# Performance work log

Measured on AMD Instinct MI355X. Metric: run time of the kernel, lower is better.

Reference implementation:

```python
import jax, jax.numpy as jnp
import numpy as np

N = 100000   # nodes
E = 1600000  # edges (avg degree 16)
F_IN = 128   # num_features
H = 128      # num_hidden
C = 40       # num_classes


def setup_inputs() -> dict:
    key = jax.random.key(0)
    ks = jax.random.split(key, 8)
    w = lambda k, sh: jax.random.normal(k, sh, dtype=jnp.float32) * 0.05
    return {
        "x": jax.random.normal(ks[0], (N, F_IN), dtype=jnp.float32),
        "edge_index": jax.random.randint(ks[1], (2, E), 0, N),
        "W_rel1": w(ks[2], (F_IN, H)),
        "b_rel1": jnp.zeros((H,), jnp.float32),
        "W_root1": w(ks[3], (F_IN, H)),
        "W_rel2": w(ks[4], (H, H)),
        "b_rel2": jnp.zeros((H,), jnp.float32),
        "W_root2": w(ks[5], (H, H)),
        "W_lin": w(ks[6], (2 * H, C)),
        "b_lin": jnp.zeros((C,), jnp.float32),
    }


def _graph_conv(x, src, dst, W_rel, b_rel, W_root, n):
    # PyG GraphConv: sum_{j in N(i)} x_j -> lin_rel, plus lin_root(x_i)
    agg = jax.ops.segment_sum(x[src], dst, num_segments=n)  # [N, d_in]
    return agg @ W_rel + b_rel + x @ W_root


def reference(x, edge_index, W_rel1, b_rel1, W_root1, W_rel2, b_rel2, W_root2, W_lin, b_lin):
    src, dst = edge_index[0], edge_index[1]
    n = x.shape[0]
    # dropout is identity at inference (training=False)
    x1 = jax.nn.relu(_graph_conv(x, src, dst, W_rel1, b_rel1, W_root1, n))
    x2 = jax.nn.relu(_graph_conv(x1, src, dst, W_rel2, b_rel2, W_root2, n))
    h = jnp.concatenate([x1, x2], axis=-1)  # [N, 2H]
    return jax.nn.log_softmax(h @ W_lin + b_lin, axis=-1)
```

## Files before the change

kernel.cpp:

```cpp
#include <hip/hip_runtime.h>
#include <hip/hip_bf16.h>

typedef __attribute__((ext_vector_type(8))) short bf16x8;
typedef __attribute__((ext_vector_type(4))) float f32x4;
typedef __attribute__((ext_vector_type(2))) float f32x2;

#define EPB 4096
#define BUCKET_BITS 8
#define BUCKET_SIZE 256
#define MAXBUCK 512

static __device__ __forceinline__ unsigned short f2bf(float f) {
    union { float f; unsigned u; } v; v.f = f;
    unsigned r = v.u + 0x7FFF + ((v.u >> 16) & 1);
    return (unsigned short)(r >> 16);
}
static __device__ __forceinline__ float asf(unsigned u) {
    union { unsigned u; float f; } v; v.u = u;
    return v.f;
}
static __device__ __forceinline__ f32x2 cvt2(unsigned u) {
    f32x2 r;
    r.x = asf(u << 16);
    r.y = asf(u & 0xFFFF0000u);
    return r;
}

__global__ __launch_bounds__(256) void prep(const float* __restrict__ Wrel1,
                                            const float* __restrict__ Wroot1,
                                            const float* __restrict__ Wrel2,
                                            const float* __restrict__ Wroot2,
                                            const float* __restrict__ Wlin,
                                            const int* __restrict__ dst,
                                            unsigned short* __restrict__ bsw1,
                                            unsigned short* __restrict__ bsw2,
                                            unsigned short* __restrict__ bswL,
                                            int* __restrict__ hist,
                                            int E, int nblk, int nbuck) {
    __shared__ int h[MAXBUCK];
    int blk = blockIdx.x, t = threadIdx.x;
    if (blk < 256) {
        const float* Wrel  = (blk < 128) ? Wrel1 : Wrel2;
        const float* Wroot = (blk < 128) ? Wroot1 : Wroot2;
        unsigned short* bsw = (blk < 128) ? bsw1 : bsw2;
        int idx = (blk & 127) * 256 + t;
        int j = idx & 7, L = (idx >> 3) & 63, ct = (idx >> 9) & 15, kt = idx >> 13;
        int k = kt * 32 + ((L >> 4) * 8) + j;
        int c = ct * 16 + (L & 15);
        float v = (c < 128) ? Wrel[k * 128 + c] : Wroot[k * 128 + (c - 128)];
        bsw[idx] = f2bf(v);
    } else if (blk < 304) {
        int idx = (blk - 256) * 256 + t;
        int tt = idx;
        int j = tt & 7; tt >>= 3;
        int L = tt & 63; tt >>= 6;
        int ct = tt % 3;
        int kt = tt / 3;
        int k = kt * 32 + ((L >> 4) * 8) + j;
        int c = ct * 16 + (L & 15);
        float v = (c < 40) ? Wlin[k * 40 + c] : 0.f;
        bswL[idx] = f2bf(v);
    } else {
        int hb = blk - 304;
        for (int i = t; i < MAXBUCK; i += 256) h[i] = 0;
        __syncthreads();
        int e0 = hb * EPB;
#pragma unroll
        for (int it = 0; it < EPB / 256; it++) {
            int e = e0 + it * 256 + t;
            if (e < E) atomicAdd(&h[dst[e] >> BUCKET_BITS], 1);
        }
        __syncthreads();
        for (int i = t; i < nbuck; i += 256) hist[i * nblk + hb] = h[i];
    }
}

__global__ __launch_bounds__(256) void bucket_total(const int* __restrict__ hist,
                                                    int* __restrict__ total, int nblk) {
    __shared__ int s[256];
    int b = blockIdx.x, t = threadIdx.x;
    int v = 0;
    for (int i = t; i < nblk; i += 256) v += hist[b * nblk + i];
    s[t] = v; __syncthreads();
#pragma unroll
    for (int o = 128; o >= 1; o >>= 1) {
        if (t < o) s[t] += s[t + o];
        __syncthreads();
    }
    if (t == 0) total[b] = s[0];
}

__global__ __launch_bounds__(256) void bucket_scan(const int* __restrict__ total,
                                                   int* __restrict__ base, int nbuck) {
    __shared__ int s[256];
    int t = threadIdx.x;
    int e0 = (2 * t < nbuck) ? total[2 * t] : 0;
    int e1 = (2 * t + 1 < nbuck) ? total[2 * t + 1] : 0;
    int ps = e0 + e1;
    s[t] = ps; __syncthreads();
#pragma unroll
    for (int o = 1; o < 256; o <<= 1) {
        int x = (t >= o) ? s[t - o] : 0;
        __syncthreads();
        s[t] += x; __syncthreads();
    }
    int pbase = s[t] - ps;
    if (2 * t <= nbuck) base[2 * t] = pbase;
    if (2 * t + 1 <= nbuck) base[2 * t + 1] = pbase + e0;
}

__global__ __launch_bounds__(256) void block_scan(int* __restrict__ hist,
                                                  const int* __restrict__ base, int nblk) {
    __shared__ int s[256];
    int b = blockIdx.x, t = threadIdx.x;
    int carryv = base[b];
    for (int start = 0; start < nblk; start += 256) {
        int i = start + t;
        int v = (i < nblk) ? hist[b * nblk + i] : 0;
        s[t] = v; __syncthreads();
#pragma unroll
        for (int o = 1; o < 256; o <<= 1) {
            int x = (t >= o) ? s[t - o] : 0;
            __syncthreads();
            s[t] += x; __syncthreads();
        }
        int excl = s[t] - v + carryv;
        if (i < nblk) hist[b * nblk + i] = excl;
        carryv += s[255];
        __syncthreads();
    }
}

__global__ __launch_bounds__(256) void edge_part(const int* __restrict__ src,
                                                 const int* __restrict__ dst,
                                                 const int* __restrict__ hist,
                                                 int* __restrict__ part,
                                                 int E, int nblk, int nbuck) {
    __shared__ int hcnt[MAXBUCK];
    __shared__ int lstart[MAXBUCK];
    __shared__ int cur[MAXBUCK];
    __shared__ int gbase[MAXBUCK];
    __shared__ int s2[256];
    __shared__ int sdst[EPB];
    __shared__ int ssrc[EPB];
    int t = threadIdx.x, blk = blockIdx.x;
    int e0 = blk * EPB;
    int cnt = E - e0; if (cnt > EPB) cnt = EPB;
    for (int i = t; i < MAXBUCK; i += 256) hcnt[i] = 0;
    for (int i = t; i < nbuck; i += 256) gbase[i] = hist[i * nblk + blk];
    __syncthreads();
    int myd[EPB / 256], mys[EPB / 256];
#pragma unroll
    for (int it = 0; it < EPB / 256; it++) {
        int i = it * 256 + t;
        if (i < cnt) {
            myd[it] = dst[e0 + i];
            mys[it] = src[e0 + i];
            atomicAdd(&hcnt[myd[it] >> BUCKET_BITS], 1);
        }
    }
    __syncthreads();
    int p0 = hcnt[2 * t], p1 = hcnt[2 * t + 1];
    int ps = p0 + p1;
    s2[t] = ps; __syncthreads();
#pragma unroll
    for (int o = 1; o < 256; o <<= 1) {
        int x = (t >= o) ? s2[t - o] : 0;
        __syncthreads();
        s2[t] += x; __syncthreads();
    }
    int pbase = s2[t] - ps;
    lstart[2 * t] = pbase; lstart[2 * t + 1] = pbase + p0;
    cur[2 * t] = 0; cur[2 * t + 1] = 0;
    __syncthreads();
#pragma unroll
    for (int it = 0; it < EPB / 256; it++) {
        int i = it * 256 + t;
        if (i < cnt) {
            int b = myd[it] >> BUCKET_BITS;
            int p = lstart[b] + atomicAdd(&cur[b], 1);
            sdst[p] = myd[it];
            ssrc[p] = mys[it];
        }
    }
    __syncthreads();
    for (int i = t; i < cnt; i += 256) {
        int d = sdst[i], s = ssrc[i];
        int b = d >> BUCKET_BITS;
        part[gbase[b] + (i - lstart[b])] = ((d & (BUCKET_SIZE - 1)) << 17) | s;
    }
}

__global__ __launch_bounds__(256) void csrfin_gemm1(const int* __restrict__ part,
                                                    const int* __restrict__ bucketBase,
                                                    int* __restrict__ off_,
                                                    int* __restrict__ deg_,
                                                    int* __restrict__ csr_src,
                                                    const float* __restrict__ x,
                                                    const unsigned short* __restrict__ Bsw,
                                                    const float* __restrict__ bias,
                                                    unsigned short* __restrict__ xr,
                                                    unsigned short* __restrict__ accbf,
                                                    int N, int nbuck) {
    __shared__ int cur[BUCKET_SIZE];
    __shared__ int h[BUCKET_SIZE];
    __shared__ int tsum[256];
    int t = threadIdx.x;
    if (blockIdx.x < (unsigned)nbuck) {
        int b = blockIdx.x;
        int lo = bucketBase[b], hi = bucketBase[b + 1];
        int n0 = b * BUCKET_SIZE;
        h[t] = 0;
        __syncthreads();
        for (int i = lo + t; i < hi; i += 256) atomicAdd(&h[part[i] >> 17], 1);
        __syncthreads();
        int hv = h[t];
        tsum[t] = hv;
        __syncthreads();
#pragma unroll
        for (int o = 1; o < 256; o <<= 1) {
            int xx = (t >= o) ? tsum[t - o] : 0;
            __syncthreads();
            tsum[t] += xx;
            __syncthreads();
        }
        int st = tsum[t] - hv;
        cur[t] = st;
        int node = n0 + t;
        if (node < N) { off_[node] = lo + st; deg_[node] = hv; }
        __syncthreads();
        for (int i = lo + t; i < hi; i += 256) {
            int rec = part[i];
            int p = atomicAdd(&cur[rec >> 17], 1);
            csr_src[lo + p] = rec & 0x1FFFF;
        }
    } else {
        int wid = (blockIdx.x - nbuck) * 4 + (t >> 6);
        int L = t & 63;
        int r0 = wid * 16;
        if (r0 >= N) return;
        int arow = r0 + (L & 15);
        const bf16x8* Bptr = ((const bf16x8*)Bsw) + L;
        f32x4 acc[16];
#pragma unroll
        for (int i = 0; i < 16; i++) acc[i] = (f32x4){0.f, 0.f, 0.f, 0.f};
#pragma unroll
        for (int kt = 0; kt < 4; kt++) {
            const float* Arow = x + (size_t)arow * 128 + ((L >> 4) * 8) + kt * 32;
            float4 a0 = *(const float4*)Arow;
            float4 a1 = *(const float4*)(Arow + 4);
            bf16x8 a;
            a[0] = (short)f2bf(a0.x); a[1] = (short)f2bf(a0.y);
            a[2] = (short)f2bf(a0.z); a[3] = (short)f2bf(a0.w);
            a[4] = (short)f2bf(a1.x); a[5] = (short)f2bf(a1.y);
            a[6] = (short)f2bf(a1.z); a[7] = (short)f2bf(a1.w);
#pragma unroll
            for (int ct = 0; ct < 16; ct++) {
                bf16x8 b = Bptr[(kt * 16 + ct) * 64];
                acc[ct] = __builtin_amdgcn_mfma_f32_16x16x32_bf16(a, b, acc[ct], 0, 0, 0);
            }
        }
        int rbase = r0 + (L >> 4) * 4;
        int cl = L & 15;
#pragma unroll
        for (int ct = 0; ct < 16; ct++) {
            int col = ct * 16 + cl;
#pragma unroll
            for (int r = 0; r < 4; r++) {
                int row = rbase + r;
                float v = acc[ct][r];
                if (col < 128)
                    xr[(size_t)row * 128 + col] = f2bf(v);
                else
                    accbf[(size_t)row * 128 + (col - 128)] = f2bf(v + bias[col - 128]);
            }
        }
    }
}

__global__ __launch_bounds__(256) void gemm_layer2(const unsigned short* __restrict__ Abf,
                                                   const unsigned short* __restrict__ Bsw,
                                                   const float* __restrict__ bias,
                                                   unsigned short* __restrict__ xr,
                                                   unsigned short* __restrict__ accbf, int N) {
    __shared__ unsigned short Bs[32768];
    int t = threadIdx.x;
    {
        uint4* d4 = (uint4*)Bs;
        const uint4* s4 = (const uint4*)Bsw;
#pragma unroll
        for (int i = 0; i < 16; i++) d4[t + i * 256] = s4[t + i * 256];
    }
    __syncthreads();
    int w = t >> 6, L = t & 63;
    int nTiles = (N + 15) / 16;
    for (int tile = blockIdx.x * 4 + w; tile < nTiles; tile += gridDim.x * 4) {
        int r0 = tile * 16;
        int arow = r0 + (L & 15);
        f32x4 acc[16];
#pragma unroll
        for (int i = 0; i < 16; i++) acc[i] = (f32x4){0.f, 0.f, 0.f, 0.f};
#pragma unroll
        for (int kt = 0; kt < 4; kt++) {
            bf16x8 a = *((const bf16x8*)(Abf + (size_t)arow * 128 + ((L >> 4) * 8) + kt * 32));
#pragma unroll
            for (int ct = 0; ct < 16; ct++) {
                bf16x8 b = *(const bf16x8*)(Bs + (((kt * 16 + ct) * 64) + L) * 8);
                acc[ct] = __builtin_amdgcn_mfma_f32_16x16x32_bf16(a, b, acc[ct], 0, 0, 0);
            }
        }
        int rbase = r0 + (L >> 4) * 4;
        int cl = L & 15;
#pragma unroll
        for (int ct = 0; ct < 16; ct++) {
            int col = ct * 16 + cl;
#pragma unroll
            for (int r = 0; r < 4; r++) {
                int row = rbase + r;
                float v = acc[ct][r];
                if (col < 128)
                    xr[(size_t)row * 128 + col] = f2bf(v);
                else
                    accbf[(size_t)row * 128 + (col - 128)] = f2bf(v + bias[col - 128]);
            }
        }
    }
}

__global__ __launch_bounds__(256) void agg_relu_cvt(const unsigned short* __restrict__ xr,
                                                    const unsigned short* __restrict__ accbf,
                                                    const int* __restrict__ off_,
                                                    const int* __restrict__ deg,
                                                    const int* __restrict__ csr_src,
                                                    unsigned short* __restrict__ out, int N) {
    int node = blockIdx.x * 4 + (threadIdx.x >> 6);
    if (node >= N) return;
    int L = threadIdx.x & 63;
    int g = L >> 4;
    int f = L & 15;
    int o = off_[node];
    int d = deg[node];
    uint4 arow = (uint4){0, 0, 0, 0};
    if (g == 0) arow = *(const uint4*)(accbf + (size_t)node * 128 + f * 8);

    const int* ip = csr_src + o + g;
    const unsigned short* xrf = xr + f * 8;

    f32x2 a0 = (f32x2){0.f, 0.f}, a1 = (f32x2){0.f, 0.f};
    f32x2 a2 = (f32x2){0.f, 0.f}, a3 = (f32x2){0.f, 0.f};

    int d4 = d & ~3;
#pragma unroll 4
    for (int k = 0; k < d4; k += 4) {
        int s = ip[k];
        uint4 p = *(const uint4*)(xrf + (size_t)s * 128);
        a0 += cvt2(p.x);
        a1 += cvt2(p.y);
        a2 += cvt2(p.z);
        a3 += cvt2(p.w);
    }
    if (d4 + g < d) {
        int s = ip[d4];
        uint4 p = *(const uint4*)(xrf + (size_t)s * 128);
        a0 += cvt2(p.x);
        a1 += cvt2(p.y);
        a2 += cvt2(p.z);
        a3 += cvt2(p.w);
    }
    a0.x += __shfl_xor(a0.x, 16, 64); a0.y += __shfl_xor(a0.y, 16, 64);
    a1.x += __shfl_xor(a1.x, 16, 64); a1.y += __shfl_xor(a1.y, 16, 64);
    a2.x += __shfl_xor(a2.x, 16, 64); a2.y += __shfl_xor(a2.y, 16, 64);
    a3.x += __shfl_xor(a3.x, 16, 64); a3.y += __shfl_xor(a3.y, 16, 64);
    a0.x += __shfl_xor(a0.x, 32, 64); a0.y += __shfl_xor(a0.y, 32, 64);
    a1.x += __shfl_xor(a1.x, 32, 64); a1.y += __shfl_xor(a1.y, 32, 64);
    a2.x += __shfl_xor(a2.x, 32, 64); a2.y += __shfl_xor(a2.y, 32, 64);
    a3.x += __shfl_xor(a3.x, 32, 64); a3.y += __shfl_xor(a3.y, 32, 64);

    if (g == 0) {
        uint4 wv;
        wv.x = ((unsigned)f2bf(fmaxf(asf(arow.x & 0xFFFF0000u) + a0.y, 0.f)) << 16)
             | f2bf(fmaxf(asf(arow.x << 16) + a0.x, 0.f));
        wv.y = ((unsigned)f2bf(fmaxf(asf(arow.y & 0xFFFF0000u) + a1.y, 0.f)) << 16)
             | f2bf(fmaxf(asf(arow.y << 16) + a1.x, 0.f));
        wv.z = ((unsigned)f2bf(fmaxf(asf(arow.z & 0xFFFF0000u) + a2.y, 0.f)) << 16)
             | f2bf(fmaxf(asf(arow.z << 16) + a2.x, 0.f));
        wv.w = ((unsigned)f2bf(fmaxf(asf(arow.w & 0xFFFF0000u) + a3.y, 0.f)) << 16)
             | f2bf(fmaxf(asf(arow.w << 16) + a3.x, 0.f));
        *(uint4*)(out + (size_t)node * 128 + f * 8) = wv;
    }
}

__global__ __launch_bounds__(256) void gemm_final_ls(const unsigned short* __restrict__ x1bf,
                                                     const unsigned short* __restrict__ x2bf,
                                                     const unsigned short* __restrict__ Bsw,
                                                     const float* __restrict__ blin,
                                                     float* __restrict__ out, int N) {
    __shared__ unsigned short Bs[12288];
    int t = threadIdx.x;
    {
        uint4* d4 = (uint4*)Bs;
        const uint4* s4 = (const uint4*)Bsw;
#pragma unroll
        for (int i = 0; i < 6; i++) d4[t + i * 256] = s4[t + i * 256];
    }
    __syncthreads();
    int w = t >> 6, L = t & 63;
    int cl = L & 15;
    float b0 = blin[cl], b1 = blin[16 + cl];
    float b2 = (cl < 8) ? blin[32 + cl] : 0.f;
    int nTiles = (N + 15) / 16;
    for (int tile = blockIdx.x * 4 + w; tile < nTiles; tile += gridDim.x * 4) {
        int r0 = tile * 16;
        int arow = r0 + (L & 15);
        f32x4 acc[3];
#pragma unroll
        for (int i = 0; i < 3; i++) acc[i] = (f32x4){0.f, 0.f, 0.f, 0.f};
#pragma unroll
        for (int kt = 0; kt < 8; kt++) {
            const unsigned short* Ab = (kt < 4) ? x1bf : x2bf;
            int kk = (kt & 3) * 32 + ((L >> 4) * 8);
            bf16x8 a = *((const bf16x8*)(Ab + (size_t)arow * 128 + kk));
#pragma unroll
            for (int ct = 0; ct < 3; ct++) {
                bf16x8 b = *(const bf16x8*)(Bs + (((kt * 3 + ct) * 64) + L) * 8);
                acc[ct] = __builtin_amdgcn_mfma_f32_16x16x32_bf16(a, b, acc[ct], 0, 0, 0);
            }
        }
        int rbase = r0 + (L >> 4) * 4;
#pragma unroll
        for (int r = 0; r < 4; r++) {
            int row = rbase + r;
            float v0 = acc[0][r] + b0;
            float v1 = acc[1][r] + b1;
            float v2 = (cl < 8) ? (acc[2][r] + b2) : -__builtin_inff();
            float m = fmaxf(fmaxf(v0, v1), v2);
#pragma unroll
            for (int off = 8; off >= 1; off >>= 1) m = fmaxf(m, __shfl_xor(m, off, 64));
            float e = __expf(v0 - m) + __expf(v1 - m) + ((cl < 8) ? __expf(v2 - m) : 0.f);
#pragma unroll
            for (int off = 8; off >= 1; off >>= 1) e += __shfl_xor(e, off, 64);
            float ls = m + __logf(e);
            float* op = out + (size_t)row * 40;
            op[cl] = v0 - ls;
            op[16 + cl] = v1 - ls;
            if (cl < 8) op[32 + cl] = v2 - ls;
        }
    }
}

extern "C" void kernel_launch(void* const* d_in, const int* in_sizes, int n_in,
                              void* d_out, int out_size, void* d_ws, size_t ws_size,
                              hipStream_t stream) {
    const float* x      = (const float*)d_in[0];
    const int*   edge   = (const int*)d_in[1];
    const float* Wrel1  = (const float*)d_in[2];
    const float* brel1  = (const float*)d_in[3];
    const float* Wroot1 = (const float*)d_in[4];
    const float* Wrel2  = (const float*)d_in[5];
    const float* brel2  = (const float*)d_in[6];
    const float* Wroot2 = (const float*)d_in[7];
    const float* Wlin   = (const float*)d_in[8];
    const float* blin   = (const float*)d_in[9];

    const int N = in_sizes[0] / 128;
    const int E = in_sizes[1] / 2;
    const int* src = edge;
    const int* dst = edge + E;

    const int nblk  = (E + EPB - 1) / EPB;
    const int nbuck = (N + BUCKET_SIZE - 1) / BUCKET_SIZE;

    char* ws = (char*)d_ws;
    size_t off = 0;
    auto alloc = [&](size_t bytes) -> void* {
        void* p = ws + off;
        off += (bytes + 255) & ~(size_t)255;
        return p;
    };
    unsigned short* x1bf = (unsigned short*)alloc((size_t)N * 128 * 2);
    unsigned short* x2bf = (unsigned short*)alloc((size_t)N * 128 * 2);
    unsigned short* xr   = (unsigned short*)alloc((size_t)N * 128 * 2);
    unsigned short* accbf= (unsigned short*)alloc((size_t)N * 128 * 2);
    unsigned short* bsw1 = (unsigned short*)alloc(32768 * 2);
    unsigned short* bsw2 = (unsigned short*)alloc(32768 * 2);
    unsigned short* bswL = (unsigned short*)alloc(12288 * 2);
    int* hist       = (int*)alloc((size_t)nbuck * nblk * 4);
    int* bucketTot  = (int*)alloc((size_t)nbuck * 4);
    int* bucketBase = (int*)alloc((size_t)(nbuck + 1) * 4);
    int* part       = (int*)alloc((size_t)E * 4);
    int* csr_src    = (int*)alloc((size_t)E * 4);
    int* off_       = (int*)alloc((size_t)N * 4);
    int* deg_       = (int*)alloc((size_t)N * 4);

    const int rowTiles = (N + 15) / 16;
    const int gemmBlocks = (rowTiles + 3) / 4;
    const int nodeBlocks = (N + 3) / 4;

    prep<<<304 + nblk, 256, 0, stream>>>(Wrel1, Wroot1, Wrel2, Wroot2, Wlin, dst,
                                         bsw1, bsw2, bswL, hist, E, nblk, nbuck);
    bucket_total<<<nbuck, 256, 0, stream>>>(hist, bucketTot, nblk);
    bucket_scan<<<1, 256, 0, stream>>>(bucketTot, bucketBase, nbuck);
    block_scan<<<nbuck, 256, 0, stream>>>(hist, bucketBase, nblk);
    edge_part<<<nblk, 256, 0, stream>>>(src, dst, hist, part, E, nblk, nbuck);
    csrfin_gemm1<<<nbuck + gemmBlocks, 256, 0, stream>>>(part, bucketBase, off_, deg_, csr_src,
                                                         x, bsw1, brel1, xr, accbf, N, nbuck);
    agg_relu_cvt<<<nodeBlocks, 256, 0, stream>>>(xr, accbf, off_, deg_, csr_src, x1bf, N);
    gemm_layer2<<<512, 256, 0, stream>>>(x1bf, bsw2, brel2, xr, accbf, N);
    agg_relu_cvt<<<nodeBlocks, 256, 0, stream>>>(xr, accbf, off_, deg_, csr_src, x2bf, N);
    gemm_final_ls<<<512, 256, 0, stream>>>(x1bf, x2bf, bswL, blin, (float*)d_out, N);
}
```

Measured before the change: 336.4 us.

## Split node range to overlap aggregation with GEMM and merge scan kernels

Each aggregation is split at the node midpoint. The second half of the aggregation runs in the same launch as the next layer's GEMM on the first half's tiles, so the gather-bound and MFMA-bound work can share the GPU. The bucket-total and two scan kernels are merged into one by adding atomic totals in the histogram pass. The edges-per-block constant is halved. Separate xr/acc buffers per layer avoid write-after-read hazards, but the agg_gemm GEMM path now reads B weights from global memory instead of LDS, and the change adds more launches plus a memset.

```diff
diff --git a/kernel.cpp b/kernel.cpp
--- a/kernel.cpp
+++ b/kernel.cpp
@@ -5,7 +5,7 @@
 typedef __attribute__((ext_vector_type(4))) float f32x4;
 typedef __attribute__((ext_vector_type(2))) float f32x2;
 
-#define EPB 4096
+#define EPB 2048
 #define BUCKET_BITS 8
 #define BUCKET_SIZE 256
 #define MAXBUCK 512
@@ -24,6 +24,154 @@
     r.x = asf(u << 16);
     r.y = asf(u & 0xFFFF0000u);
     return r;
+}
+
+
+static __device__ __forceinline__ void dev_agg(int node, int L,
+                                               const unsigned short* __restrict__ xr,
+                                               const unsigned short* __restrict__ accbf,
+                                               const int* __restrict__ off_,
+                                               const int* __restrict__ deg,
+                                               const int* __restrict__ csr_src,
+                                               unsigned short* __restrict__ out) {
+    int g = L >> 4;
+    int f = L & 15;
+    int o = off_[node];
+    int d = deg[node];
+    uint4 arow = (uint4){0, 0, 0, 0};
+    if (g == 0) arow = *(const uint4*)(accbf + (size_t)node * 128 + f * 8);
+
+    const int* ip = csr_src + o + g;
+    const unsigned short* xrf = xr + f * 8;
+
+    f32x2 a0 = (f32x2){0.f, 0.f}, a1 = (f32x2){0.f, 0.f};
+    f32x2 a2 = (f32x2){0.f, 0.f}, a3 = (f32x2){0.f, 0.f};
+
+    int d4 = d & ~3;
+#pragma unroll 4
+    for (int k = 0; k < d4; k += 4) {
+        int s = ip[k];
+        uint4 p = *(const uint4*)(xrf + (size_t)s * 128);
+        a0 += cvt2(p.x);
+        a1 += cvt2(p.y);
+        a2 += cvt2(p.z);
+        a3 += cvt2(p.w);
+    }
+    if (d4 + g < d) {
+        int s = ip[d4];
+        uint4 p = *(const uint4*)(xrf + (size_t)s * 128);
+        a0 += cvt2(p.x);
+        a1 += cvt2(p.y);
+        a2 += cvt2(p.z);
+        a3 += cvt2(p.w);
+    }
+    a0.x += __shfl_xor(a0.x, 16, 64); a0.y += __shfl_xor(a0.y, 16, 64);
+    a1.x += __shfl_xor(a1.x, 16, 64); a1.y += __shfl_xor(a1.y, 16, 64);
+    a2.x += __shfl_xor(a2.x, 16, 64); a2.y += __shfl_xor(a2.y, 16, 64);
+    a3.x += __shfl_xor(a3.x, 16, 64); a3.y += __shfl_xor(a3.y, 16, 64);
+    a0.x += __shfl_xor(a0.x, 32, 64); a0.y += __shfl_xor(a0.y, 32, 64);
+    a1.x += __shfl_xor(a1.x, 32, 64); a1.y += __shfl_xor(a1.y, 32, 64);
+    a2.x += __shfl_xor(a2.x, 32, 64); a2.y += __shfl_xor(a2.y, 32, 64);
+    a3.x += __shfl_xor(a3.x, 32, 64); a3.y += __shfl_xor(a3.y, 32, 64);
+
+    if (g == 0) {
+        uint4 wv;
+        wv.x = ((unsigned)f2bf(fmaxf(asf(arow.x & 0xFFFF0000u) + a0.y, 0.f)) << 16)
+             | f2bf(fmaxf(asf(arow.x << 16) + a0.x, 0.f));
+        wv.y = ((unsigned)f2bf(fmaxf(asf(arow.y & 0xFFFF0000u) + a1.y, 0.f)) << 16)
+             | f2bf(fmaxf(asf(arow.y << 16) + a1.x, 0.f));
+        wv.z = ((unsigned)f2bf(fmaxf(asf(arow.z & 0xFFFF0000u) + a2.y, 0.f)) << 16)
+             | f2bf(fmaxf(asf(arow.z << 16) + a2.x, 0.f));
+        wv.w = ((unsigned)f2bf(fmaxf(asf(arow.w & 0xFFFF0000u) + a3.y, 0.f)) << 16)
+             | f2bf(fmaxf(asf(arow.w << 16) + a3.x, 0.f));
+        *(uint4*)(out + (size_t)node * 128 + f * 8) = wv;
+    }
+}
+
+static __device__ __forceinline__ void dev_gemm_tile(int tile, int L,
+                                                     const unsigned short* __restrict__ Abf,
+                                                     const unsigned short* Bsrc,
+                                                     const float* __restrict__ bias,
+                                                     unsigned short* __restrict__ xrO,
+                                                     unsigned short* __restrict__ accO, int N) {
+    int r0 = tile * 16;
+    if (r0 >= N) return;
+    int arow = r0 + (L & 15);
+    const bf16x8* Bptr = ((const bf16x8*)Bsrc) + L;
+    f32x4 acc[16];
+#pragma unroll
+    for (int i = 0; i < 16; i++) acc[i] = (f32x4){0.f, 0.f, 0.f, 0.f};
+#pragma unroll
+    for (int kt = 0; kt < 4; kt++) {
+        bf16x8 a = *((const bf16x8*)(Abf + (size_t)arow * 128 + ((L >> 4) * 8) + kt * 32));
+#pragma unroll
+        for (int ct = 0; ct < 16; ct++) {
+            bf16x8 b = Bptr[(kt * 16 + ct) * 64];
+            acc[ct] = __builtin_amdgcn_mfma_f32_16x16x32_bf16(a, b, acc[ct], 0, 0, 0);
+        }
+    }
+    int rbase = r0 + (L >> 4) * 4;
+    int cl = L & 15;
+#pragma unroll
+    for (int ct = 0; ct < 16; ct++) {
+        int col = ct * 16 + cl;
+#pragma unroll
+        for (int r = 0; r < 4; r++) {
+            int row = rbase + r;
+            float v = acc[ct][r];
+            if (col < 128)
+                xrO[(size_t)row * 128 + col] = f2bf(v);
+            else
+                accO[(size_t)row * 128 + (col - 128)] = f2bf(v + bias[col - 128]);
+        }
+    }
+}
+
+static __device__ __forceinline__ void dev_final_tile(int tile, int L,
+                                                      const unsigned short* __restrict__ x1bf,
+                                                      const unsigned short* __restrict__ x2bf,
+                                                      const unsigned short* Bsrc,
+                                                      const float* __restrict__ blin,
+                                                      float* __restrict__ out, int N) {
+    int r0 = tile * 16;
+    if (r0 >= N) return;
+    int arow = r0 + (L & 15);
+    f32x4 acc[3];
+#pragma unroll
+    for (int i = 0; i < 3; i++) acc[i] = (f32x4){0.f, 0.f, 0.f, 0.f};
+#pragma unroll
+    for (int kt = 0; kt < 8; kt++) {
+        const unsigned short* Ab = (kt < 4) ? x1bf : x2bf;
+        int kk = (kt & 3) * 32 + ((L >> 4) * 8);
+        bf16x8 a = *((const bf16x8*)(Ab + (size_t)arow * 128 + kk));
+#pragma unroll
+        for (int ct = 0; ct < 3; ct++) {
+            bf16x8 b = ((const bf16x8*)Bsrc)[(kt * 3 + ct) * 64 + L];
+            acc[ct] = __builtin_amdgcn_mfma_f32_16x16x32_bf16(a, b, acc[ct], 0, 0, 0);
+        }
+    }
+    int rbase = r0 + (L >> 4) * 4;
+    int cl = L & 15;
+    float b0 = blin[cl], b1 = blin[16 + cl];
+    float b2 = (cl < 8) ? blin[32 + cl] : 0.f;
+#pragma unroll
+    for (int r = 0; r < 4; r++) {
+        int row = rbase + r;
+        float v0 = acc[0][r] + b0;
+        float v1 = acc[1][r] + b1;
+        float v2 = (cl < 8) ? (acc[2][r] + b2) : -__builtin_inff();
+        float m = fmaxf(fmaxf(v0, v1), v2);
+#pragma unroll
+        for (int off = 8; off >= 1; off >>= 1) m = fmaxf(m, __shfl_xor(m, off, 64));
+        float e = __expf(v0 - m) + __expf(v1 - m) + ((cl < 8) ? __expf(v2 - m) : 0.f);
+#pragma unroll
+        for (int off = 8; off >= 1; off >>= 1) e += __shfl_xor(e, off, 64);
+        float ls = m + __logf(e);
+        float* op = out + (size_t)row * 40;
+        op[cl] = v0 - ls;
+        op[16 + cl] = v1 - ls;
+        if (cl < 8) op[32 + cl] = v2 - ls;
+    }
 }
 
 __global__ __launch_bounds__(256) void prep(const float* __restrict__ Wrel1,
@@ -36,6 +184,7 @@
                                             unsigned short* __restrict__ bsw2,
                                             unsigned short* __restrict__ bswL,
                                             int* __restrict__ hist,
+                                            int* __restrict__ bucketTot,
                                             int E, int nblk, int nbuck) {
     __shared__ int h[MAXBUCK];
     int blk = blockIdx.x, t = threadIdx.x;
@@ -71,31 +220,23 @@
             if (e < E) atomicAdd(&h[dst[e] >> BUCKET_BITS], 1);
         }
         __syncthreads();
-        for (int i = t; i < nbuck; i += 256) hist[i * nblk + hb] = h[i];
-    }
-}
-
-__global__ __launch_bounds__(256) void bucket_total(const int* __restrict__ hist,
-                                                    int* __restrict__ total, int nblk) {
+        for (int i = t; i < nbuck; i += 256) {
+            int v = h[i];
+            hist[i * nblk + hb] = v;
+            if (v) atomicAdd(&bucketTot[i], v);
+        }
+    }
+}
+
+__global__ __launch_bounds__(256) void scan2(int* __restrict__ hist,
+                                             const int* __restrict__ bucketTot,
+                                             int* __restrict__ bucketBase,
+                                             int nblk, int nbuck, int E) {
     __shared__ int s[256];
+    __shared__ int bases[MAXBUCK];
     int b = blockIdx.x, t = threadIdx.x;
-    int v = 0;
-    for (int i = t; i < nblk; i += 256) v += hist[b * nblk + i];
-    s[t] = v; __syncthreads();
-#pragma unroll
-    for (int o = 128; o >= 1; o >>= 1) {
-        if (t < o) s[t] += s[t + o];
-        __syncthreads();
-    }
-    if (t == 0) total[b] = s[0];
-}
-
-__global__ __launch_bounds__(256) void bucket_scan(const int* __restrict__ total,
-                                                   int* __restrict__ base, int nbuck) {
-    __shared__ int s[256];
-    int t = threadIdx.x;
-    int e0 = (2 * t < nbuck) ? total[2 * t] : 0;
-    int e1 = (2 * t + 1 < nbuck) ? total[2 * t + 1] : 0;
+    int e0 = (2 * t < nbuck) ? bucketTot[2 * t] : 0;
+    int e1 = (2 * t + 1 < nbuck) ? bucketTot[2 * t + 1] : 0;
     int ps = e0 + e1;
     s[t] = ps; __syncthreads();
 #pragma unroll
@@ -105,18 +246,19 @@
         s[t] += x; __syncthreads();
     }
     int pbase = s[t] - ps;
-    if (2 * t <= nbuck) base[2 * t] = pbase;
-    if (2 * t + 1 <= nbuck) base[2 * t + 1] = pbase + e0;
-}
-
-__global__ __launch_bounds__(256) void block_scan(int* __restrict__ hist,
-                                                  const int* __restrict__ base, int nblk) {
-    __shared__ int s[256];
-    int b = blockIdx.x, t = threadIdx.x;
-    int carryv = base[b];
+    bases[2 * t] = pbase;
+    bases[2 * t + 1] = pbase + e0;
+    __syncthreads();
+    int base_b = bases[b];
+    if (t == 0) {
+        bucketBase[b] = base_b;
+        if (b == 0) bucketBase[nbuck] = E;
+    }
+    int carryv = base_b;
     for (int start = 0; start < nblk; start += 256) {
         int i = start + t;
         int v = (i < nblk) ? hist[b * nblk + i] : 0;
+        __syncthreads();
         s[t] = v; __syncthreads();
 #pragma unroll
         for (int o = 1; o < 256; o <<= 1) {
@@ -127,7 +269,6 @@
         int excl = s[t] - v + carryv;
         if (i < nblk) hist[b * nblk + i] = excl;
         carryv += s[255];
-        __syncthreads();
     }
 }
 
@@ -278,11 +419,70 @@
     }
 }
 
-__global__ __launch_bounds__(256) void gemm_layer2(const unsigned short* __restrict__ Abf,
-                                                   const unsigned short* __restrict__ Bsw,
-                                                   const float* __restrict__ bias,
-                                                   unsigned short* __restrict__ xr,
-                                                   unsigned short* __restrict__ accbf, int N) {
+__global__ __launch_bounds__(256) void agg_k(const unsigned short* __restrict__ xr,
+                                             const unsigned short* __restrict__ accbf,
+                                             const int* __restrict__ off_,
+                                             const int* __restrict__ deg,
+                                             const int* __restrict__ csr_src,
+                                             unsigned short* __restrict__ out,
+                                             int node0, int nNodes) {
+    int rel = blockIdx.x * 4 + (threadIdx.x >> 6);
+    if (rel >= nNodes) return;
+    dev_agg(node0 + rel, threadIdx.x & 63, xr, accbf, off_, deg, csr_src, out);
+}
+
+__global__ __launch_bounds__(256) void agg_gemm(const unsigned short* __restrict__ xr,
+                                                const unsigned short* __restrict__ accbf,
+                                                const int* __restrict__ off_,
+                                                const int* __restrict__ deg,
+                                                const int* __restrict__ csr_src,
+                                                unsigned short* __restrict__ aggOut,
+                                                int aggNode0, int aggNodes, int aggBlocks,
+                                                const unsigned short* __restrict__ Abf,
+                                                const unsigned short* __restrict__ Bsw,
+                                                const float* __restrict__ bias,
+                                                unsigned short* __restrict__ xrO,
+                                                unsigned short* __restrict__ accO,
+                                                int nTilesA, int N) {
+    int t = threadIdx.x;
+    if ((int)blockIdx.x < aggBlocks) {
+        int rel = blockIdx.x * 4 + (t >> 6);
+        if (rel < aggNodes) dev_agg(aggNode0 + rel, t & 63, xr, accbf, off_, deg, csr_src, aggOut);
+    } else {
+        int wid = (blockIdx.x - aggBlocks) * 4 + (t >> 6);
+        if (wid < nTilesA) dev_gemm_tile(wid, t & 63, Abf, Bsw, bias, xrO, accO, N);
+    }
+}
+
+__global__ __launch_bounds__(256) void agg_final(const unsigned short* __restrict__ xr,
+                                                 const unsigned short* __restrict__ accbf,
+                                                 const int* __restrict__ off_,
+                                                 const int* __restrict__ deg,
+                                                 const int* __restrict__ csr_src,
+                                                 unsigned short* __restrict__ aggOut,
+                                                 int aggNode0, int aggNodes, int aggBlocks,
+                                                 const unsigned short* __restrict__ x1bf,
+                                                 const unsigned short* __restrict__ x2bf,
+                                                 const unsigned short* __restrict__ bswL,
+                                                 const float* __restrict__ blin,
+                                                 float* __restrict__ out,
+                                                 int nTilesA, int N) {
+    int t = threadIdx.x;
+    if ((int)blockIdx.x < aggBlocks) {
+        int rel = blockIdx.x * 4 + (t >> 6);
+        if (rel < aggNodes) dev_agg(aggNode0 + rel, t & 63, xr, accbf, off_, deg, csr_src, aggOut);
+    } else {
+        int wid = (blockIdx.x - aggBlocks) * 4 + (t >> 6);
+        if (wid < nTilesA) dev_final_tile(wid, t & 63, x1bf, x2bf, bswL, blin, out, N);
+    }
+}
+
+__global__ __launch_bounds__(256) void gemm_layer_rng(const unsigned short* __restrict__ Abf,
+                                                      const unsigned short* __restrict__ Bsw,
+                                                      const float* __restrict__ bias,
+                                                      unsigned short* __restrict__ xrO,
+                                                      unsigned short* __restrict__ accO,
+                                                      int tile0, int tileEnd, int N) {
     __shared__ unsigned short Bs[32768];
     int t = threadIdx.x;
     {
@@ -293,159 +493,28 @@
     }
     __syncthreads();
     int w = t >> 6, L = t & 63;
-    int nTiles = (N + 15) / 16;
-    for (int tile = blockIdx.x * 4 + w; tile < nTiles; tile += gridDim.x * 4) {
-        int r0 = tile * 16;
-        int arow = r0 + (L & 15);
-        f32x4 acc[16];
-#pragma unroll
-        for (int i = 0; i < 16; i++) acc[i] = (f32x4){0.f, 0.f, 0.f, 0.f};
-#pragma unroll
-        for (int kt = 0; kt < 4; kt++) {
-            bf16x8 a = *((const bf16x8*)(Abf + (size_t)arow * 128 + ((L >> 4) * 8) + kt * 32));
-#pragma unroll
-            for (int ct = 0; ct < 16; ct++) {
-                bf16x8 b = *(const bf16x8*)(Bs + (((kt * 16 + ct) * 64) + L) * 8);
-                acc[ct] = __builtin_amdgcn_mfma_f32_16x16x32_bf16(a, b, acc[ct], 0, 0, 0);
-            }
-        }
-        int rbase = r0 + (L >> 4) * 4;
-        int cl = L & 15;
-#pragma unroll
-        for (int ct = 0; ct < 16; ct++) {
-            int col = ct * 16 + cl;
-#pragma unroll
-            for (int r = 0; r < 4; r++) {
-                int row = rbase + r;
-                float v = acc[ct][r];
-                if (col < 128)
-                    xr[(size_t)row * 128 + col] = f2bf(v);
-                else
-                    accbf[(size_t)row * 128 + (col - 128)] = f2bf(v + bias[col - 128]);
-            }
-        }
-    }
-}
-
-__global__ __launch_bounds__(256) void agg_relu_cvt(const unsigned short* __restrict__ xr,
-                                                    const unsigned short* __restrict__ accbf,
-                                                    const int* __restrict__ off_,
-                                                    const int* __restrict__ deg,
-                                                    const int* __restrict__ csr_src,
-                                                    unsigned short* __restrict__ out, int N) {
-    int node = blockIdx.x * 4 + (threadIdx.x >> 6);
-    if (node >= N) return;
-    int L = threadIdx.x & 63;
-    int g = L >> 4;
-    int f = L & 15;
-    int o = off_[node];
-    int d = deg[node];
-    uint4 arow = (uint4){0, 0, 0, 0};
-    if (g == 0) arow = *(const uint4*)(accbf + (size_t)node * 128 + f * 8);
-
-    const int* ip = csr_src + o + g;
-    const unsigned short* xrf = xr + f * 8;
-
-    f32x2 a0 = (f32x2){0.f, 0.f}, a1 = (f32x2){0.f, 0.f};
-    f32x2 a2 = (f32x2){0.f, 0.f}, a3 = (f32x2){0.f, 0.f};
-
-    int d4 = d & ~3;
-#pragma unroll 4
-    for (int k = 0; k < d4; k += 4) {
-        int s = ip[k];
-        uint4 p = *(const uint4*)(xrf + (size_t)s * 128);
-        a0 += cvt2(p.x);
-        a1 += cvt2(p.y);
-        a2 += cvt2(p.z);
-        a3 += cvt2(p.w);
-    }
-    if (d4 + g < d) {
-        int s = ip[d4];
-        uint4 p = *(const uint4*)(xrf + (size_t)s * 128);
-        a0 += cvt2(p.x);
-        a1 += cvt2(p.y);
-        a2 += cvt2(p.z);
-        a3 += cvt2(p.w);
-    }
-    a0.x += __shfl_xor(a0.x, 16, 64); a0.y += __shfl_xor(a0.y, 16, 64);
-    a1.x += __shfl_xor(a1.x, 16, 64); a1.y += __shfl_xor(a1.y, 16, 64);
-    a2.x += __shfl_xor(a2.x, 16, 64); a2.y += __shfl_xor(a2.y, 16, 64);
-    a3.x += __shfl_xor(a3.x, 16, 64); a3.y += __shfl_xor(a3.y, 16, 64);
-    a0.x += __shfl_xor(a0.x, 32, 64); a0.y += __shfl_xor(a0.y, 32, 64);
-    a1.x += __shfl_xor(a1.x, 32, 64); a1.y += __shfl_xor(a1.y, 32, 64);
-    a2.x += __shfl_xor(a2.x, 32, 64); a2.y += __shfl_xor(a2.y, 32, 64);
-    a3.x += __shfl_xor(a3.x, 32, 64); a3.y += __shfl_xor(a3.y, 32, 64);
-
-    if (g == 0) {
-        uint4 wv;
-        wv.x = ((unsigned)f2bf(fmaxf(asf(arow.x & 0xFFFF0000u) + a0.y, 0.f)) << 16)
-             | f2bf(fmaxf(asf(arow.x << 16) + a0.x, 0.f));
-        wv.y = ((unsigned)f2bf(fmaxf(asf(arow.y & 0xFFFF0000u) + a1.y, 0.f)) << 16)
-             | f2bf(fmaxf(asf(arow.y << 16) + a1.x, 0.f));
-        wv.z = ((unsigned)f2bf(fmaxf(asf(arow.z & 0xFFFF0000u) + a2.y, 0.f)) << 16)
-             | f2bf(fmaxf(asf(arow.z << 16) + a2.x, 0.f));
-        wv.w = ((unsigned)f2bf(fmaxf(asf(arow.w & 0xFFFF0000u) + a3.y, 0.f)) << 16)
-             | f2bf(fmaxf(asf(arow.w << 16) + a3.x, 0.f));
-        *(uint4*)(out + (size_t)node * 128 + f * 8) = wv;
-    }
-}
-
-__global__ __launch_bounds__(256) void gemm_final_ls(const unsigned short* __restrict__ x1bf,
-                                                     const unsigned short* __restrict__ x2bf,
-                                                     const unsigned short* __restrict__ Bsw,
-                                                     const float* __restrict__ blin,
-                                                     float* __restrict__ out, int N) {
+    for (int tile = tile0 + blockIdx.x * 4 + w; tile < tileEnd; tile += gridDim.x * 4)
+        dev_gemm_tile(tile, L, Abf, Bs, bias, xrO, accO, N);
+}
+
+__global__ __launch_bounds__(256) void final_rng(const unsigned short* __restrict__ x1bf,
+                                                 const unsigned short* __restrict__ x2bf,
+                                                 const unsigned short* __restrict__ bswL,
+                                                 const float* __restrict__ blin,
+                                                 float* __restrict__ out,
+                                                 int tile0, int tileEnd, int N) {
     __shared__ unsigned short Bs[12288];
     int t = threadIdx.x;
     {
         uint4* d4 = (uint4*)Bs;
-        const uint4* s4 = (const uint4*)Bsw;
+        const uint4* s4 = (const uint4*)bswL;
 #pragma unroll
         for (int i = 0; i < 6; i++) d4[t + i * 256] = s4[t + i * 256];
     }
     __syncthreads();
     int w = t >> 6, L = t & 63;
-    int cl = L & 15;
-    float b0 = blin[cl], b1 = blin[16 + cl];
-    float b2 = (cl < 8) ? blin[32 + cl] : 0.f;
-    int nTiles = (N + 15) / 16;
-    for (int tile = blockIdx.x * 4 + w; tile < nTiles; tile += gridDim.x * 4) {
-        int r0 = tile * 16;
-        int arow = r0 + (L & 15);
-        f32x4 acc[3];
-#pragma unroll
-        for (int i = 0; i < 3; i++) acc[i] = (f32x4){0.f, 0.f, 0.f, 0.f};
-#pragma unroll
-        for (int kt = 0; kt < 8; kt++) {
-            const unsigned short* Ab = (kt < 4) ? x1bf : x2bf;
-            int kk = (kt & 3) * 32 + ((L >> 4) * 8);
-            bf16x8 a = *((const bf16x8*)(Ab + (size_t)arow * 128 + kk));
-#pragma unroll
-            for (int ct = 0; ct < 3; ct++) {
-                bf16x8 b = *(const bf16x8*)(Bs + (((kt * 3 + ct) * 64) + L) * 8);
-                acc[ct] = __builtin_amdgcn_mfma_f32_16x16x32_bf16(a, b, acc[ct], 0, 0, 0);
-            }
-        }
-        int rbase = r0 + (L >> 4) * 4;
-#pragma unroll
-        for (int r = 0; r < 4; r++) {
-            int row = rbase + r;
-            float v0 = acc[0][r] + b0;
-            float v1 = acc[1][r] + b1;
-            float v2 = (cl < 8) ? (acc[2][r] + b2) : -__builtin_inff();
-            float m = fmaxf(fmaxf(v0, v1), v2);
-#pragma unroll
-            for (int off = 8; off >= 1; off >>= 1) m = fmaxf(m, __shfl_xor(m, off, 64));
-            float e = __expf(v0 - m) + __expf(v1 - m) + ((cl < 8) ? __expf(v2 - m) : 0.f);
-#pragma unroll
-            for (int off = 8; off >= 1; off >>= 1) e += __shfl_xor(e, off, 64);
-            float ls = m + __logf(e);
-            float* op = out + (size_t)row * 40;
-            op[cl] = v0 - ls;
-            op[16 + cl] = v1 - ls;
-            if (cl < 8) op[32 + cl] = v2 - ls;
-        }
-    }
+    for (int tile = tile0 + blockIdx.x * 4 + w; tile < tileEnd; tile += gridDim.x * 4)
+        dev_final_tile(tile, L, x1bf, x2bf, Bs, blin, out, N);
 }
 
 extern "C" void kernel_launch(void* const* d_in, const int* in_sizes, int n_in,
@@ -479,8 +548,10 @@
     };
     unsigned short* x1bf = (unsigned short*)alloc((size_t)N * 128 * 2);
     unsigned short* x2bf = (unsigned short*)alloc((size_t)N * 128 * 2);
-    unsigned short* xr   = (unsigned short*)alloc((size_t)N * 128 * 2);
-    unsigned short* accbf= (unsigned short*)alloc((size_t)N * 128 * 2);
+    unsigned short* xr1  = (unsigned short*)alloc((size_t)N * 128 * 2);
+    unsigned short* acc1 = (unsigned short*)alloc((size_t)N * 128 * 2);
+    unsigned short* xr2  = (unsigned short*)alloc((size_t)N * 128 * 2);
+    unsigned short* acc2 = (unsigned short*)alloc((size_t)N * 128 * 2);
     unsigned short* bsw1 = (unsigned short*)alloc(32768 * 2);
     unsigned short* bsw2 = (unsigned short*)alloc(32768 * 2);
     unsigned short* bswL = (unsigned short*)alloc(12288 * 2);
@@ -492,20 +563,32 @@
     int* off_       = (int*)alloc((size_t)N * 4);
     int* deg_       = (int*)alloc((size_t)N * 4);
 
-    const int rowTiles = (N + 15) / 16;
-    const int gemmBlocks = (rowTiles + 3) / 4;
-    const int nodeBlocks = (N + 3) / 4;
-
+    const int tilesTotal = (N + 15) / 16;
+    const int gemmBlocksFull = (tilesTotal + 3) / 4;
+    const int halfN = ((N / 2) / 16) * 16;
+    const int nodesB = N - halfN;
+    const int aggBlocksA = (halfN + 3) / 4;
+    const int aggBlocksB = (nodesB + 3) / 4;
+    const int tilesA = halfN / 16;
+    const int gemmABlocks = (tilesA + 3) / 4;
+
+    hipMemsetAsync(bucketTot, 0, (size_t)nbuck * 4, stream);
     prep<<<304 + nblk, 256, 0, stream>>>(Wrel1, Wroot1, Wrel2, Wroot2, Wlin, dst,
-                                         bsw1, bsw2, bswL, hist, E, nblk, nbuck);
-    bucket_total<<<nbuck, 256, 0, stream>>>(hist, bucketTot, nblk);
-    bucket_scan<<<1, 256, 0, stream>>>(bucketTot, bucketBase, nbuck);
-    block_scan<<<nbuck, 256, 0, stream>>>(hist, bucketBase, nblk);
+                                         bsw1, bsw2, bswL, hist, bucketTot, E, nblk, nbuck);
+    scan2<<<nbuck, 256, 0, stream>>>(hist, bucketTot, bucketBase, nblk, nbuck, E);
     edge_part<<<nblk, 256, 0, stream>>>(src, dst, hist, part, E, nblk, nbuck);
-    csrfin_gemm1<<<nbuck + gemmBlocks, 256, 0, stream>>>(part, bucketBase, off_, deg_, csr_src,
-                                                         x, bsw1, brel1, xr, accbf, N, nbuck);
-    agg_relu_cvt<<<nodeBlocks, 256, 0, stream>>>(xr, accbf, off_, deg_, csr_src, x1bf, N);
-    gemm_layer2<<<512, 256, 0, stream>>>(x1bf, bsw2, brel2, xr, accbf, N);
-    agg_relu_cvt<<<nodeBlocks, 256, 0, stream>>>(xr, accbf, off_, deg_, csr_src, x2bf, N);
-    gemm_final_ls<<<512, 256, 0, stream>>>(x1bf, x2bf, bswL, blin, (float*)d_out, N);
-}
+    csrfin_gemm1<<<nbuck + gemmBlocksFull, 256, 0, stream>>>(part, bucketBase, off_, deg_, csr_src,
+                                                             x, bsw1, brel1, xr1, acc1, N, nbuck);
+    agg_k<<<aggBlocksA, 256, 0, stream>>>(xr1, acc1, off_, deg_, csr_src, x1bf, 0, halfN);
+    agg_gemm<<<aggBlocksB + gemmABlocks, 256, 0, stream>>>(xr1, acc1, off_, deg_, csr_src, x1bf,
+                                                           halfN, nodesB, aggBlocksB,
+                                                           x1bf, bsw2, brel2, xr2, acc2, tilesA, N);
+    gemm_layer_rng<<<512, 256, 0, stream>>>(x1bf, bsw2, brel2, xr2, acc2, tilesA, tilesTotal, N);
+    agg_k<<<aggBlocksA, 256, 0, stream>>>(xr2, acc2, off_, deg_, csr_src, x2bf, 0, halfN);
+    agg_final<<<aggBlocksB + gemmABlocks, 256, 0, stream>>>(xr2, acc2, off_, deg_, csr_src, x2bf,
+                                                            halfN, nodesB, aggBlocksB,
+                                                            x1bf, x2bf, bswL, blin, (float*)d_out,
+                                                            tilesA, N);
+    final_rng<<<512, 256, 0, stream>>>(x1bf, x2bf, bswL, blin, (float*)d_out,
+                                       tilesA, tilesTotal, N);
+}
```

Result: slower. 413.3 us (+22.9%).
